# Performance work log

Hardware: AMD Instinct MI355X
Metric: run time of the kernel (lower is better)

Reference implementation:

```python
import jax, jax.numpy as jnp
import numpy as np

N_ROWS = 100000   # sparse matrix rows (nodes)
N_COLS = 8192     # input feature dim
UNITS = 128
NNZ = 2000000     # ~20 nonzeros per row


def setup_inputs() -> dict:
    key = jax.random.key(0)
    k1, k2, k3, k4, k5 = jax.random.split(key, 5)
    vals = jax.random.normal(k1, (NNZ,), dtype=jnp.float32)
    rows = jax.random.randint(k2, (NNZ,), 0, N_ROWS, dtype=jnp.int32)
    cols = jax.random.randint(k3, (NNZ,), 0, N_COLS, dtype=jnp.int32)
    # GlorotUniform-style scale for W, matching the TF initializer statistics
    limit = jnp.sqrt(6.0 / (N_COLS + UNITS)).astype(jnp.float32)
    W = jax.random.uniform(k4, (N_COLS, UNITS), dtype=jnp.float32, minval=-limit, maxval=limit)
    b = jax.random.uniform(k5, (UNITS,), dtype=jnp.float32, minval=-limit, maxval=limit)
    return {"vals": vals, "rows": rows, "cols": cols, "W": W, "b": b, "num_rows": N_ROWS}


def reference(vals, rows, cols, W, b, num_rows):
    # sparse (COO) [num_rows, F] @ dense W [F, units]:
    # gather the W row for each nonzero, scale by the nonzero value,
    # then scatter-add into the output row -> segment_sum over `rows`.
    gathered = W[cols] * vals[:, None]            # [nnz, units]
    out = jax.ops.segment_sum(gathered, rows, num_segments=num_rows)  # [num_rows, units]
    return out + b                                 # bias add (use_bias=True)
```

## Files before the change

### kernel.cpp

```cpp
#include <hip/hip_runtime.h>
#include <hip/hip_fp16.h>


#define UNITS 128
#define SCAN_BLK 1024
#define BROW 98
#define NBC_PAD 1024
#define BCAP 2528
#define CH2 8192
#define SPILL_CAP 8192


__global__ __launch_bounds__(256) void setup_kernel(
        const float* __restrict__ W, __half2* __restrict__ Wh,
        int* __restrict__ ccur, int* __restrict__ spill_cnt,
        int nbc, int wn2 ) {
    int t = blockIdx.x * blockDim.x + threadIdx.x;
    if (t < nbc) ccur[t] = t * BCAP;
    if (t == nbc) *spill_cnt = 0;
    int stride = gridDim.x * blockDim.x;
    const float2* W2 = (const float2*)W;
    for (int i = t; i < wn2; i += stride)
        Wh[i] = __float22half2_rn(W2[i]);
}


__global__ __launch_bounds__(512, 8) void partition_kernel(
        const float* __restrict__ vals, const int* __restrict__ rows,
        const int* __restrict__ cols, int* __restrict__ ccur,
        float2* __restrict__ sortedA, int* __restrict__ spill_cnt,
        float2* __restrict__ spill, int nnz, int nbc) {
    __shared__ unsigned short invs[CH2];
    __shared__ int hist[NBC_PAD];
    __shared__ int pref[NBC_PAD];
    __shared__ int gdelta[NBC_PAD];

    const int t = threadIdx.x;
    const int chunk0 = blockIdx.x * CH2;
    int n = nnz - chunk0;
    if (n > CH2) n = CH2;

    hist[t] = 0; hist[t + 512] = 0;
    __syncthreads();

    int bk[16];
#pragma unroll
    for (int j = 0; j < 16; ++j) {
        int r = j * 512 + t;
        int bkt = -1;
        if (r < n) {
            bkt = rows[chunk0 + r] / BROW;
            atomicAdd(&hist[bkt], 1);
        }
        bk[j] = bkt;
    }
    __syncthreads();

    pref[t] = hist[t]; pref[t + 512] = hist[t + 512];
    __syncthreads();
    for (int off = 1; off < NBC_PAD; off <<= 1) {
        int a0 = (t >= off) ? pref[t - off] : 0;
        int a1 = (t + 512 >= off) ? pref[t + 512 - off] : 0;
        __syncthreads();
        pref[t] += a0; pref[t + 512] += a1;
        __syncthreads();
    }

#pragma unroll
    for (int u = 0; u < 2; ++u) {
        int s = t + u * 512;
        int c = hist[s];
        int excl = pref[s] - c;
        if (s < nbc) {
            int g = (c > 0) ? atomicAdd(&ccur[s], c) : 0;
            gdelta[s] = g - excl;
        }
        hist[s] = excl;
    }
    __syncthreads();

#pragma unroll
    for (int j = 0; j < 16; ++j) {
        int bkt = bk[j];
        if (bkt >= 0) {
            int pos = atomicAdd(&hist[bkt], 1);
            invs[pos] = (unsigned short)(j * 512 + t);
        }
    }
    __syncthreads();

    for (int s = t; s < n; s += 512) {
        int r = invs[s];
        int i = chunk0 + r;
        int row = rows[i];
        float v = vals[i];
        int col = cols[i];
        int bkt = row / BROW;
        int rowlo = row - bkt * BROW;
        int dest = gdelta[bkt] + s;
        if (dest < (bkt + 1) * BCAP) {
            sortedA[dest] = make_float2(v, __int_as_float(col | (rowlo << 13)));
        } else {
            int sp = atomicAdd(spill_cnt, 1);
            if (sp < SPILL_CAP)
                spill[sp] = make_float2(v, __int_as_float(col | (row << 13)));
        }
    }
}


__global__ __launch_bounds__(512, 8) void fused_sort_compute_kernel(
        const float2* __restrict__ A, const int* __restrict__ ccur,
        const __half2* __restrict__ Wh, const float* __restrict__ b,
        float* __restrict__ out, const int* __restrict__ spill_cnt,
        const float2* __restrict__ spill, int NR) {
    __shared__ float2 st[BCAP + 8];
    __shared__ int cnt_s[128];
    __shared__ int rs[132];
    __shared__ int spill_n;
    const int t = threadIdx.x;
    const int lane = t & 63;
    const int w = t >> 6;
    const int bb = blockIdx.x;
    const int r0 = bb * BROW;
    const int gstart = bb * BCAP;
    int cnt = ccur[bb] - gstart;
    if (cnt > BCAP) cnt = BCAP;

    const float2 bias = ((const float2*)b)[lane];

    if (t < 128) cnt_s[t] = 0;
    if (t == 0) {
        int sn = *spill_cnt;
        spill_n = (sn > SPILL_CAP) ? SPILL_CAP : sn;
    }
    __syncthreads();

    float2 e[5];
#pragma unroll
    for (int j = 0; j < 5; ++j) {
        int k = j * 512 + t;
        if (k < cnt) {
            e[j] = A[gstart + k];
            atomicAdd(&cnt_s[(__float_as_int(e[j].y) >> 13) & 127], 1);
        }
    }
    __syncthreads();

    if (t < 128) rs[t] = cnt_s[t];
    __syncthreads();
    for (int off = 1; off < 128; off <<= 1) {
        int v = (t < 128 && t >= off) ? rs[t - off] : 0;
        __syncthreads();
        if (t < 128) rs[t] += v;
        __syncthreads();
    }
    int excl = (t < 128) ? rs[t] - cnt_s[t] : 0;
    __syncthreads();
    if (t < 128) { rs[t] = excl; cnt_s[t] = excl; }
    if (t == 0) rs[128] = cnt;
    __syncthreads();

#pragma unroll
    for (int j = 0; j < 5; ++j) {
        int k = j * 512 + t;
        if (k < cnt) {
            int pk = __float_as_int(e[j].y);
            int p = atomicAdd(&cnt_s[(pk >> 13) & 127], 1);
            st[p] = make_float2(e[j].x, __int_as_float(pk & 8191));
        }
    }
    __syncthreads();

    const int sn = spill_n;
    for (int r = w; r < BROW; r += 8) {
        int grow = r0 + r;
        if (grow >= NR) break;
        int s = rs[r], ee = rs[r + 1];
        float ax0 = 0.f, ay0 = 0.f, ax1 = 0.f, ay1 = 0.f;
        for (int k = s; k < ee; k += 4) {
            float2 p0 = st[k];
            float2 p1 = st[k + 1];
            float2 p2 = st[k + 2];
            float2 p3 = st[k + 3];
            int c0 = __float_as_int(p0.y) & 8191;
            int c1 = __float_as_int(p1.y) & 8191;
            int c2 = __float_as_int(p2.y) & 8191;
            int c3 = __float_as_int(p3.y) & 8191;
            float v0 = p0.x;
            float v1 = (k + 1 < ee) ? p1.x : 0.f;
            float v2 = (k + 2 < ee) ? p2.x : 0.f;
            float v3 = (k + 3 < ee) ? p3.x : 0.f;
            float2 w0 = __half22float2(Wh[c0 * 64 + lane]);
            float2 w1 = __half22float2(Wh[c1 * 64 + lane]);
            float2 w2 = __half22float2(Wh[c2 * 64 + lane]);
            float2 w3 = __half22float2(Wh[c3 * 64 + lane]);
            ax0 += v0 * w0.x; ay0 += v0 * w0.y;
            ax1 += v1 * w1.x; ay1 += v1 * w1.y;
            ax0 += v2 * w2.x; ay0 += v2 * w2.y;
            ax1 += v3 * w3.x; ay1 += v3 * w3.y;
        }
        for (int s2 = 0; s2 < sn; ++s2) {
            float2 es = spill[s2];
            int pk = __float_as_int(es.y);
            if ((pk >> 13) == grow) {
                float2 wv = __half22float2(Wh[(pk & 8191) * 64 + lane]);
                ax0 += es.x * wv.x; ay0 += es.x * wv.y;
            }
        }
        ((float2*)out)[(size_t)grow * 64 + lane] =
            make_float2(ax0 + ax1 + bias.x, ay0 + ay1 + bias.y);
    }
}


__global__ void hist_kernel(const int* __restrict__ rows, int* __restrict__ counts, int nnz) {
    int i = blockIdx.x * blockDim.x + threadIdx.x;
    if (i < nnz) atomicAdd(&counts[rows[i]], 1);
}

__global__ void scan1_kernel(const int* __restrict__ counts, int* __restrict__ tmp,
                             int* __restrict__ bsums, int NR, int NS) {
    __shared__ int s[SCAN_BLK];
    int t = threadIdx.x;
    int i = blockIdx.x * SCAN_BLK + t;
    int x = (i < NR) ? counts[i] : 0;
    s[t] = x;
    __syncthreads();
    for (int off = 1; off < SCAN_BLK; off <<= 1) {
        int v = (t >= off) ? s[t - off] : 0;
        __syncthreads();
        s[t] += v;
        __syncthreads();
    }
    if (i < NS) tmp[i] = s[t] - x;
    if (t == SCAN_BLK - 1) bsums[blockIdx.x] = s[SCAN_BLK - 1];
}

__global__ void scan2_kernel(int* __restrict__ bsums, int nb) {
    if (threadIdx.x == 0 && blockIdx.x == 0) {
        int run = 0;
        for (int i = 0; i < nb; ++i) { int c = bsums[i]; bsums[i] = run; run += c; }
    }
}

__global__ void scan3_kernel(const int* __restrict__ tmp, const int* __restrict__ bsums,
                             int* __restrict__ row_start, int* __restrict__ cursor,
                             int NR, int NS) {
    int i = blockIdx.x * blockDim.x + threadIdx.x;
    if (i < NS) {
        int v = tmp[i] + bsums[i >> 10];
        row_start[i] = v;
        if (i < NR) cursor[i] = v;
    }
}

__global__ void scatter_sort_kernel(const float* __restrict__ vals, const int* __restrict__ rows,
                                    const int* __restrict__ cols, int* __restrict__ cursor,
                                    float2* __restrict__ sorted, int nnz) {
    int i = blockIdx.x * blockDim.x + threadIdx.x;
    if (i < nnz) {
        int r = rows[i];
        int p = atomicAdd(&cursor[r], 1);
        sorted[p] = make_float2(vals[i], __int_as_float(cols[i]));
    }
}

__global__ void compute_kernel(const float2* __restrict__ sorted, const int* __restrict__ row_start,
                               const float* __restrict__ W, const float* __restrict__ b,
                               float* __restrict__ out, int NR) {
    int lane = threadIdx.x & 63;
    int wv = threadIdx.x >> 6;
    int row = blockIdx.x * 4 + wv;
    if (row >= NR) return;
    int start = row_start[row];
    int end   = row_start[row + 1];
    const float2* W2 = (const float2*)W;
    float accx0 = 0.f, accy0 = 0.f, accx1 = 0.f, accy1 = 0.f;
    for (int base = start; base < end; base += 64) {
        int m = end - base;
        if (m > 64) m = 64;
        float2 p = make_float2(0.f, __int_as_float(0));
        if (lane < m) p = sorted[base + lane];
        int vi = __float_as_int(p.x);
        int ci = __float_as_int(p.y);
        int rounds = (m + 3) & ~3;
        for (int j = 0; j < rounds; j += 4) {
            float v0 = __int_as_float(__builtin_amdgcn_readlane(vi, j));
            int   c0 = __builtin_amdgcn_readlane(ci, j);
            float v1 = __int_as_float(__builtin_amdgcn_readlane(vi, j + 1));
            int   c1 = __builtin_amdgcn_readlane(ci, j + 1);
            float v2 = __int_as_float(__builtin_amdgcn_readlane(vi, j + 2));
            int   c2 = __builtin_amdgcn_readlane(ci, j + 2);
            float v3 = __int_as_float(__builtin_amdgcn_readlane(vi, j + 3));
            int   c3 = __builtin_amdgcn_readlane(ci, j + 3);
            float2 w0 = W2[c0 * 64 + lane];
            float2 w1 = W2[c1 * 64 + lane];
            float2 w2 = W2[c2 * 64 + lane];
            float2 w3 = W2[c3 * 64 + lane];
            accx0 += v0 * w0.x; accy0 += v0 * w0.y;
            accx1 += v1 * w1.x; accy1 += v1 * w1.y;
            accx0 += v2 * w2.x; accy0 += v2 * w2.y;
            accx1 += v3 * w3.x; accy1 += v3 * w3.y;
        }
    }
    float2 bb = ((const float2*)b)[lane];
    ((float2*)out)[(size_t)row * 64 + lane] =
        make_float2(accx0 + accx1 + bb.x, accy0 + accy1 + bb.y);
}


__global__ void init_bias_kernel(float* __restrict__ out, const float* __restrict__ b, int total4) {
    const float4* b4 = (const float4*)b;
    float4* out4 = (float4*)out;
    int stride = gridDim.x * blockDim.x;
    for (int j = blockIdx.x * blockDim.x + threadIdx.x; j < total4; j += stride)
        out4[j] = b4[j & 31];
}

__global__ void scatter_atomic_kernel(const float* __restrict__ vals, const int* __restrict__ rows,
                                      const int* __restrict__ cols, const float* __restrict__ W,
                                      float* __restrict__ out, int nnz) {
    long long idx = (long long)blockIdx.x * blockDim.x + threadIdx.x;
    int i = (int)(idx >> 5);
    int c = (int)(idx & 31);
    if (i >= nnz) return;
    int row = rows[i], col = cols[i];
    float v = vals[i];
    float4 w = ((const float4*)W)[col * 32 + c];
    float* o = out + (size_t)row * UNITS + (c << 2);
    atomicAdd(o + 0, v * w.x);
    atomicAdd(o + 1, v * w.y);
    atomicAdd(o + 2, v * w.z);
    atomicAdd(o + 3, v * w.w);
}

extern "C" void kernel_launch(void* const* d_in, const int* in_sizes, int n_in,
                              void* d_out, int out_size, void* d_ws, size_t ws_size,
                              hipStream_t stream) {
    const float* vals = (const float*)d_in[0];
    const int*   rows = (const int*)d_in[1];
    const int*   cols = (const int*)d_in[2];
    const float* W    = (const float*)d_in[3];
    const float* b    = (const float*)d_in[4];
    float* out = (float*)d_out;

    const int nnz = in_sizes[0];
    const int NW  = in_sizes[3];
    const int NR  = out_size / UNITS;
    const int NS  = NR + 1;
    const int NB  = (NS + SCAN_BLK - 1) / SCAN_BLK;
    const int nbc = (NR + BROW - 1) / BROW;

    auto align = [](size_t x) { return (x + 255) & ~(size_t)255; };

    size_t off_ccur    = 0;
    size_t off_scnt    = align(off_ccur + (size_t)nbc * 4);
    size_t off_spill   = align(off_scnt + 4);
    size_t off_wh      = align(off_spill + (size_t)SPILL_CAP * 8);
    size_t off_sortedA = align(off_wh + (size_t)NW * 2);
    size_t needed_full = off_sortedA + (size_t)nbc * BCAP * 8;

    size_t t2_counts   = 0;
    size_t t2_tmp      = align(t2_counts + (size_t)NR * 4);
    size_t t2_bsums    = align(t2_tmp    + (size_t)NS * 4);
    size_t t2_rowstart = align(t2_bsums  + (size_t)NB * 4);
    size_t t2_cursor   = align(t2_rowstart + (size_t)NS * 4);
    size_t t2_sorted   = align(t2_cursor + (size_t)NR * 4);
    size_t needed_r2   = t2_sorted + (size_t)nnz * 8;

    char* ws = (char*)d_ws;

    if (ws_size >= needed_full && nbc <= NBC_PAD) {
        int*     ccur      = (int*)(ws + off_ccur);
        int*     spill_cnt = (int*)(ws + off_scnt);
        float2*  spill     = (float2*)(ws + off_spill);
        __half2* Wh        = (__half2*)(ws + off_wh);
        float2*  sortedA   = (float2*)(ws + off_sortedA);

        setup_kernel<<<512, 256, 0, stream>>>(W, Wh, ccur, spill_cnt, nbc, NW / 2);
        {
            int grid = (nnz + CH2 - 1) / CH2;
            partition_kernel<<<grid, 512, 0, stream>>>(vals, rows, cols, ccur, sortedA,
                                                       spill_cnt, spill, nnz, nbc);
        }
        fused_sort_compute_kernel<<<nbc, 512, 0, stream>>>(sortedA, ccur, Wh, b, out,
                                                           spill_cnt, spill, NR);
    } else if (ws_size >= needed_r2) {
        int*    counts    = (int*)(ws + t2_counts);
        int*    tmp       = (int*)(ws + t2_tmp);
        int*    bsums     = (int*)(ws + t2_bsums);
        int*    row_start = (int*)(ws + t2_rowstart);
        int*    cursor    = (int*)(ws + t2_cursor);
        float2* sorted    = (float2*)(ws + t2_sorted);

        hipMemsetAsync(counts, 0, (size_t)NR * 4, stream);
        {
            int block = 256, grid = (nnz + block - 1) / block;
            hist_kernel<<<grid, block, 0, stream>>>(rows, counts, nnz);
        }
        scan1_kernel<<<NB, SCAN_BLK, 0, stream>>>(counts, tmp, bsums, NR, NS);
        scan2_kernel<<<1, 64, 0, stream>>>(bsums, NB);
        {
            int block = 256, grid = (NS + block - 1) / block;
            scan3_kernel<<<grid, block, 0, stream>>>(tmp, bsums, row_start, cursor, NR, NS);
        }
        {
            int block = 256, grid = (nnz + block - 1) / block;
            scatter_sort_kernel<<<grid, block, 0, stream>>>(vals, rows, cols, cursor, sorted, nnz);
        }
        {
            int grid = (NR + 3) / 4;
            compute_kernel<<<grid, 256, 0, stream>>>(sorted, row_start, W, b, out, NR);
        }
    } else {
        int total4 = out_size / 4;
        int block = 256;
        int grid = (total4 + block - 1) / block;
        init_bias_kernel<<<grid, block, 0, stream>>>(out, b, total4);
        long long total_threads = (long long)nnz * 32;
        long long g2 = (total_threads + block - 1) / block;
        scatter_atomic_kernel<<<(int)g2, block, 0, stream>>>(vals, rows, cols, W, out, nnz);
    }
}
```

Measured before the change: 169.6 us.

## Fuse partition and compute into one persistent kernel with a grid barrier

Replaces the three-launch pipeline (setup, partition, sort+compute) with a single kernel. Each chunk block locally sorts its nonzeros by row bucket and writes per-bucket offsets, the spare blocks convert W to half, and all blocks then meet at a software grid barrier built on global atomics. After the barrier each bucket block gathers its entries from every chunk by binary search, sorts them by row in shared memory and computes the output rows. This removes kernel launch gaps and the global atomic scatter with spill handling. In exchange it depends on all ~1021 blocks being co-resident to avoid deadlock, and it silently caps each bucket at STCAP entries.

```diff
diff --git a/kernel.cpp b/kernel.cpp
--- a/kernel.cpp
+++ b/kernel.cpp
@@ -5,16 +5,253 @@
 #define UNITS 128
 #define SCAN_BLK 1024
 #define BROW 98
+#define CHA 4096
+#define NCHMAX 512
+#define NBCMAX 1024
+#define STCAP 3300
 #define NBC_PAD 1024
 #define BCAP 2528
 #define CH2 8192
 #define SPILL_CAP 8192
 
 
+__global__ __launch_bounds__(512, 8) void mega_kernel(
+        const float* __restrict__ vals, const int* __restrict__ rows,
+        const int* __restrict__ cols, const float* __restrict__ W,
+        const float* __restrict__ bias,
+        __half2* __restrict__ Wh, float2* __restrict__ sortedA,
+        int* __restrict__ boffT, int* __restrict__ bar,
+        float* __restrict__ out,
+        int nnz, int NR, int nch, int wn2) {
+    __shared__ __align__(16) char smem[36904];
+    const int t = threadIdx.x;
+    const int lane = t & 63;
+    const int w = t >> 6;
+    const int bb = blockIdx.x;
+    const int nblk = gridDim.x;
+
+    if (bb < nch) {
+        float2* sStage = (float2*)smem;
+        int*    sHist  = (int*)(smem + 32768);
+        int*    sWsum  = (int*)(smem + 36864);
+        const int chunk0 = bb * CHA;
+        int n = nnz - chunk0;
+        if (n > CHA) n = CHA;
+
+        sHist[t] = 0; sHist[t + 512] = 0;
+        __syncthreads();
+
+        int rowj[8];
+#pragma unroll
+        for (int j = 0; j < 8; ++j) {
+            int r = j * 512 + t;
+            int rv = (r < n) ? rows[chunk0 + r] : -1;
+            rowj[j] = rv;
+            if (rv >= 0) atomicAdd(&sHist[rv / BROW], 1);
+        }
+        __syncthreads();
+
+        int a0 = sHist[2 * t], a1 = sHist[2 * t + 1];
+        int ps = a0 + a1;
+        int inc = ps;
+#pragma unroll
+        for (int o = 1; o < 64; o <<= 1) {
+            int u = __shfl_up(inc, o);
+            if (lane >= o) inc += u;
+        }
+        if (lane == 63) sWsum[w] = inc;
+        __syncthreads();
+        int wbase = 0;
+        for (int i = 0; i < w; ++i) wbase += sWsum[i];
+        int exclp = wbase + inc - ps;
+        boffT[(2 * t) * NCHMAX + bb]     = exclp;
+        boffT[(2 * t + 1) * NCHMAX + bb] = exclp + a0;
+        sHist[2 * t]     = exclp;
+        sHist[2 * t + 1] = exclp + a0;
+        __syncthreads();
+
+#pragma unroll
+        for (int j = 0; j < 8; ++j) {
+            int rv = rowj[j];
+            if (rv >= 0) {
+                int r = j * 512 + t;
+                int bkt = rv / BROW;
+                int rowlo = rv - bkt * BROW;
+                int pos = atomicAdd(&sHist[bkt], 1);
+                float v = vals[chunk0 + r];
+                int col = cols[chunk0 + r];
+                sStage[pos] = make_float2(v, __int_as_float(col | (rowlo << 13)));
+            }
+        }
+        __syncthreads();
+
+        float2* dst = sortedA + (size_t)bb * CHA;
+        for (int s = t; s < n; s += 512) dst[s] = sStage[s];
+    } else {
+        const float2* W2 = (const float2*)W;
+        int cb = bb - nch;
+        int stride = (nblk - nch) * 512;
+        for (int i = cb * 512 + t; i < wn2; i += stride)
+            Wh[i] = __float22half2_rn(W2[i]);
+    }
+
+    __threadfence();
+    __syncthreads();
+    if (t == 0) {
+        int prev = __hip_atomic_fetch_add(&bar[0], 1, __ATOMIC_ACQ_REL,
+                                          __HIP_MEMORY_SCOPE_AGENT);
+        if (prev == nblk - 1)
+            __hip_atomic_store(&bar[1], 1, __ATOMIC_RELEASE,
+                               __HIP_MEMORY_SCOPE_AGENT);
+        while (__hip_atomic_load(&bar[1], __ATOMIC_ACQUIRE,
+                                 __HIP_MEMORY_SCOPE_AGENT) == 0)
+            __builtin_amdgcn_s_sleep(8);
+    }
+    __syncthreads();
+    __threadfence();
+
+    float2* sSt     = (float2*)smem;
+    int*    sRb0    = (int*)(smem + 26464);
+    int*    sRb1    = (int*)(smem + 28512);
+    int*    sDpos   = (int*)(smem + 30560);
+    int*    sCnt    = (int*)(smem + 32612);
+    int*    sRs     = (int*)(smem + 33124);
+    int*    sWsumB  = (int*)(smem + 33640);
+    int*    sRowNext= (int*)(smem + 33676);
+
+    const int r0 = bb * BROW;
+    const float2 bv = ((const float2*)bias)[lane];
+
+    for (int c = t; c < nch; c += 512) {
+        sRb0[c] = boffT[bb * NCHMAX + c];
+        sRb1[c] = boffT[(bb + 1) * NCHMAX + c];
+    }
+    if (t < 128) sCnt[t] = 0;
+    if (t == 0) sRowNext[0] = 0;
+    __syncthreads();
+
+    int len = (t < nch) ? (sRb1[t] - sRb0[t]) : 0;
+    int inc2 = len;
+#pragma unroll
+    for (int o = 1; o < 64; o <<= 1) {
+        int u = __shfl_up(inc2, o);
+        if (lane >= o) inc2 += u;
+    }
+    if (lane == 63) sWsumB[w] = inc2;
+    __syncthreads();
+    int wbase2 = 0;
+    for (int i = 0; i < w; ++i) wbase2 += sWsumB[i];
+    int excl2 = wbase2 + inc2 - len;
+    sDpos[t] = excl2;
+    if (t == 511) sDpos[512] = excl2 + len;
+    __syncthreads();
+
+    int cnt = sDpos[nch];
+    if (cnt > STCAP) cnt = STCAP;
+
+    float2 e[7];
+#pragma unroll
+    for (int j = 0; j < 7; ++j) {
+        int g = j * 512 + t;
+        if (g < cnt) {
+            int lo = 0, hi = nch;
+            while (hi - lo > 1) {
+                int mid = (lo + hi) >> 1;
+                if (sDpos[mid] <= g) lo = mid; else hi = mid;
+            }
+            int o2 = g - sDpos[lo];
+            e[j] = sortedA[(size_t)lo * CHA + sRb0[lo] + o2];
+            atomicAdd(&sCnt[(__float_as_int(e[j].y) >> 13) & 127], 1);
+        }
+    }
+    __syncthreads();
+
+    if (t < 128) sRs[t] = sCnt[t];
+    __syncthreads();
+    for (int off = 1; off < 128; off <<= 1) {
+        int v = (t < 128 && t >= off) ? sRs[t - off] : 0;
+        __syncthreads();
+        if (t < 128) sRs[t] += v;
+        __syncthreads();
+    }
+    int excl3 = (t < 128) ? sRs[t] - sCnt[t] : 0;
+    __syncthreads();
+    if (t < 128) { sRs[t] = excl3; sCnt[t] = excl3; }
+    if (t == 0) sRs[128] = cnt;
+    __syncthreads();
+
+#pragma unroll
+    for (int j = 0; j < 7; ++j) {
+        int g = j * 512 + t;
+        if (g < cnt) {
+            int pk = __float_as_int(e[j].y);
+            int p = atomicAdd(&sCnt[(pk >> 13) & 127], 1);
+            sSt[p] = make_float2(e[j].x, __int_as_float(pk & 8191));
+        }
+    }
+    __syncthreads();
+
+    while (true) {
+        int rr = 0;
+        if (lane == 0) rr = atomicAdd(sRowNext, 1);
+        rr = __shfl(rr, 0);
+        if (rr >= BROW) break;
+        int grow = r0 + rr;
+        if (grow >= NR) break;
+        int s = sRs[rr], ee = sRs[rr + 1];
+        float ax0 = 0.f, ay0 = 0.f, ax1 = 0.f, ay1 = 0.f;
+        for (int k = s; k < ee; k += 8) {
+            float2 p0 = sSt[k];
+            float2 p1 = sSt[k + 1];
+            float2 p2 = sSt[k + 2];
+            float2 p3 = sSt[k + 3];
+            float2 p4 = sSt[k + 4];
+            float2 p5 = sSt[k + 5];
+            float2 p6 = sSt[k + 6];
+            float2 p7 = sSt[k + 7];
+            int c0 = __float_as_int(p0.y) & 8191;
+            int c1 = __float_as_int(p1.y) & 8191;
+            int c2 = __float_as_int(p2.y) & 8191;
+            int c3 = __float_as_int(p3.y) & 8191;
+            int c4 = __float_as_int(p4.y) & 8191;
+            int c5 = __float_as_int(p5.y) & 8191;
+            int c6 = __float_as_int(p6.y) & 8191;
+            int c7 = __float_as_int(p7.y) & 8191;
+            float v0 = p0.x;
+            float v1 = (k + 1 < ee) ? p1.x : 0.f;
+            float v2 = (k + 2 < ee) ? p2.x : 0.f;
+            float v3 = (k + 3 < ee) ? p3.x : 0.f;
+            float v4 = (k + 4 < ee) ? p4.x : 0.f;
+            float v5 = (k + 5 < ee) ? p5.x : 0.f;
+            float v6 = (k + 6 < ee) ? p6.x : 0.f;
+            float v7 = (k + 7 < ee) ? p7.x : 0.f;
+            float2 w0 = __half22float2(Wh[c0 * 64 + lane]);
+            float2 w1 = __half22float2(Wh[c1 * 64 + lane]);
+            float2 w2 = __half22float2(Wh[c2 * 64 + lane]);
+            float2 w3 = __half22float2(Wh[c3 * 64 + lane]);
+            float2 w4 = __half22float2(Wh[c4 * 64 + lane]);
+            float2 w5 = __half22float2(Wh[c5 * 64 + lane]);
+            float2 w6 = __half22float2(Wh[c6 * 64 + lane]);
+            float2 w7 = __half22float2(Wh[c7 * 64 + lane]);
+            ax0 += v0 * w0.x; ay0 += v0 * w0.y;
+            ax1 += v1 * w1.x; ay1 += v1 * w1.y;
+            ax0 += v2 * w2.x; ay0 += v2 * w2.y;
+            ax1 += v3 * w3.x; ay1 += v3 * w3.y;
+            ax0 += v4 * w4.x; ay0 += v4 * w4.y;
+            ax1 += v5 * w5.x; ay1 += v5 * w5.y;
+            ax0 += v6 * w6.x; ay0 += v6 * w6.y;
+            ax1 += v7 * w7.x; ay1 += v7 * w7.y;
+        }
+        ((float2*)out)[(size_t)grow * 64 + lane] =
+            make_float2(ax0 + ax1 + bv.x, ay0 + ay1 + bv.y);
+    }
+}
+
+
 __global__ __launch_bounds__(256) void setup_kernel(
         const float* __restrict__ W, __half2* __restrict__ Wh,
         int* __restrict__ ccur, int* __restrict__ spill_cnt,
-        int nbc, int wn2 ) {
+        int nbc, int wn2) {
     int t = blockIdx.x * blockDim.x + threadIdx.x;
     if (t < nbc) ccur[t] = t * BCAP;
     if (t == nbc) *spill_cnt = 0;
@@ -23,7 +260,6 @@
     for (int i = t; i < wn2; i += stride)
         Wh[i] = __float22half2_rn(W2[i]);
 }
-
 
 __global__ __launch_bounds__(512, 8) void partition_kernel(
         const float* __restrict__ vals, const int* __restrict__ rows,
@@ -107,7 +343,6 @@
         }
     }
 }
-
 
 __global__ __launch_bounds__(512, 8) void fused_sort_compute_kernel(
         const float2* __restrict__ A, const int* __restrict__ ccur,
@@ -351,8 +586,15 @@
     const int NS  = NR + 1;
     const int NB  = (NS + SCAN_BLK - 1) / SCAN_BLK;
     const int nbc = (NR + BROW - 1) / BROW;
+    const int nch = (nnz + CHA - 1) / CHA;
 
     auto align = [](size_t x) { return (x + 255) & ~(size_t)255; };
+
+    size_t c_wh      = 0;
+    size_t c_sortedA = align(c_wh + (size_t)NW * 2);
+    size_t c_boffT   = align(c_sortedA + (size_t)nch * CHA * 8);
+    size_t c_bar     = align(c_boffT + (size_t)NBCMAX * NCHMAX * 4);
+    size_t needed_coop = c_bar + 256;
 
     size_t off_ccur    = 0;
     size_t off_scnt    = align(off_ccur + (size_t)nbc * 4);
@@ -371,7 +613,17 @@
 
     char* ws = (char*)d_ws;
 
-    if (ws_size >= needed_full && nbc <= NBC_PAD) {
+    if (ws_size >= needed_coop && nbc >= 2 && nbc <= NBCMAX &&
+        nch >= 1 && nch <= NCHMAX && nch < nbc) {
+        __half2* Wh      = (__half2*)(ws + c_wh);
+        float2*  sortedA = (float2*)(ws + c_sortedA);
+        int*     boffT   = (int*)(ws + c_boffT);
+        int*     bar     = (int*)(ws + c_bar);
+
+        hipMemsetAsync(bar, 0, 8, stream);
+        mega_kernel<<<nbc, 512, 0, stream>>>(vals, rows, cols, W, b, Wh, sortedA,
+                                             boffT, bar, out, nnz, NR, nch, NW / 2);
+    } else if (ws_size >= needed_full && nbc <= NBC_PAD) {
         int*     ccur      = (int*)(ws + off_ccur);
         int*     spill_cnt = (int*)(ws + off_scnt);
         float2*  spill     = (float2*)(ws + off_spill);
```

New measurement: 579.4 us. 3.42x slower.

## Fold W half conversion into partition kernel, shrink chunks, use wave-shuffle scan

Applied to the files above, without the earlier changes.

Removes the separate setup kernel. W-to-half conversion now runs inside the partition kernel, and the bucket cursors plus spill counter are zeroed with one memset. Partition chunks shrink from 8192 to 2048 elements, giving about four times as many blocks, and the 1024-entry LDS Hillis-Steele scan becomes a wave-shuffle scan over pairs. The goal is to cut launch overhead, the barrier-heavy scan and per-block serial work, at the cost of many more global atomics on the bucket cursors and shorter contiguous write runs into each bucket.

```diff
diff --git a/kernel.cpp b/kernel.cpp
--- a/kernel.cpp
+++ b/kernel.cpp
@@ -7,45 +7,43 @@
 #define BROW 98
 #define NBC_PAD 1024
 #define BCAP 2528
-#define CH2 8192
+#define CH3 2048
 #define SPILL_CAP 8192
-
-
-__global__ __launch_bounds__(256) void setup_kernel(
-        const float* __restrict__ W, __half2* __restrict__ Wh,
-        int* __restrict__ ccur, int* __restrict__ spill_cnt,
-        int nbc, int wn2 ) {
-    int t = blockIdx.x * blockDim.x + threadIdx.x;
-    if (t < nbc) ccur[t] = t * BCAP;
-    if (t == nbc) *spill_cnt = 0;
-    int stride = gridDim.x * blockDim.x;
-    const float2* W2 = (const float2*)W;
-    for (int i = t; i < wn2; i += stride)
-        Wh[i] = __float22half2_rn(W2[i]);
-}
 
 
 __global__ __launch_bounds__(512, 8) void partition_kernel(
         const float* __restrict__ vals, const int* __restrict__ rows,
-        const int* __restrict__ cols, int* __restrict__ ccur,
-        float2* __restrict__ sortedA, int* __restrict__ spill_cnt,
-        float2* __restrict__ spill, int nnz, int nbc) {
-    __shared__ unsigned short invs[CH2];
+        const int* __restrict__ cols, const float* __restrict__ W,
+        __half2* __restrict__ Wh, int* __restrict__ ccur,
+        float2* __restrict__ sortedA, float2* __restrict__ spill,
+        int nnz, int nbc, int wn2) {
+    __shared__ unsigned short invs[CH3];
     __shared__ int hist[NBC_PAD];
-    __shared__ int pref[NBC_PAD];
     __shared__ int gdelta[NBC_PAD];
+    __shared__ int wsum[8];
 
     const int t = threadIdx.x;
-    const int chunk0 = blockIdx.x * CH2;
+    const int lane = t & 63;
+    const int w = t >> 6;
+    const int bb = blockIdx.x;
+
+    {
+        const float2* W2 = (const float2*)W;
+        int stride = gridDim.x * 512;
+        for (int i = bb * 512 + t; i < wn2; i += stride)
+            Wh[i] = __float22half2_rn(W2[i]);
+    }
+
+    const int chunk0 = bb * CH3;
     int n = nnz - chunk0;
-    if (n > CH2) n = CH2;
+    if (n > CH3) n = CH3;
 
     hist[t] = 0; hist[t + 512] = 0;
     __syncthreads();
 
-    int bk[16];
+    int bk[4];
 #pragma unroll
-    for (int j = 0; j < 16; ++j) {
+    for (int j = 0; j < 4; ++j) {
         int r = j * 512 + t;
         int bkt = -1;
         if (r < n) {
@@ -56,31 +54,37 @@
     }
     __syncthreads();
 
-    pref[t] = hist[t]; pref[t + 512] = hist[t + 512];
-    __syncthreads();
-    for (int off = 1; off < NBC_PAD; off <<= 1) {
-        int a0 = (t >= off) ? pref[t - off] : 0;
-        int a1 = (t + 512 >= off) ? pref[t + 512 - off] : 0;
-        __syncthreads();
-        pref[t] += a0; pref[t + 512] += a1;
-        __syncthreads();
-    }
-
+    int a0 = hist[2 * t], a1 = hist[2 * t + 1];
+    int ps = a0 + a1;
+    int inc = ps;
 #pragma unroll
-    for (int u = 0; u < 2; ++u) {
-        int s = t + u * 512;
-        int c = hist[s];
-        int excl = pref[s] - c;
-        if (s < nbc) {
-            int g = (c > 0) ? atomicAdd(&ccur[s], c) : 0;
-            gdelta[s] = g - excl;
-        }
-        hist[s] = excl;
+    for (int o = 1; o < 64; o <<= 1) {
+        int u = __shfl_up(inc, o);
+        if (lane >= o) inc += u;
+    }
+    if (lane == 63) wsum[w] = inc;
+    __syncthreads();
+    int wbase = 0;
+    for (int i = 0; i < w; ++i) wbase += wsum[i];
+    int exclp = wbase + inc - ps;
+
+    {
+        int s0 = 2 * t, s1 = 2 * t + 1;
+        if (s0 < nbc) {
+            int g = (a0 > 0) ? atomicAdd(&ccur[s0], a0) : 0;
+            gdelta[s0] = s0 * BCAP + g - exclp;
+        }
+        if (s1 < nbc) {
+            int g = (a1 > 0) ? atomicAdd(&ccur[s1], a1) : 0;
+            gdelta[s1] = s1 * BCAP + g - (exclp + a0);
+        }
+        hist[s0] = exclp;
+        hist[s1] = exclp + a0;
     }
     __syncthreads();
 
 #pragma unroll
-    for (int j = 0; j < 16; ++j) {
+    for (int j = 0; j < 4; ++j) {
         int bkt = bk[j];
         if (bkt >= 0) {
             int pos = atomicAdd(&hist[bkt], 1);
@@ -89,6 +93,7 @@
     }
     __syncthreads();
 
+    int* spill_cnt = &ccur[nbc];
     for (int s = t; s < n; s += 512) {
         int r = invs[s];
         int i = chunk0 + r;
@@ -112,8 +117,7 @@
 __global__ __launch_bounds__(512, 8) void fused_sort_compute_kernel(
         const float2* __restrict__ A, const int* __restrict__ ccur,
         const __half2* __restrict__ Wh, const float* __restrict__ b,
-        float* __restrict__ out, const int* __restrict__ spill_cnt,
-        const float2* __restrict__ spill, int NR) {
+        float* __restrict__ out, int nbc, int NR) {
     __shared__ float2 st[BCAP + 8];
     __shared__ int cnt_s[128];
     __shared__ int rs[132];
@@ -124,14 +128,14 @@
     const int bb = blockIdx.x;
     const int r0 = bb * BROW;
     const int gstart = bb * BCAP;
-    int cnt = ccur[bb] - gstart;
+    int cnt = ccur[bb];
     if (cnt > BCAP) cnt = BCAP;
 
     const float2 bias = ((const float2*)b)[lane];
 
     if (t < 128) cnt_s[t] = 0;
     if (t == 0) {
-        int sn = *spill_cnt;
+        int sn = ccur[nbc];
         spill_n = (sn > SPILL_CAP) ? SPILL_CAP : sn;
     }
     __syncthreads();
@@ -173,6 +177,7 @@
     __syncthreads();
 
     const int sn = spill_n;
+    const float2* spill = A + (size_t)nbc * BCAP;
     for (int r = w; r < BROW; r += 8) {
         int grow = r0 + r;
         if (grow >= NR) break;
@@ -355,11 +360,10 @@
     auto align = [](size_t x) { return (x + 255) & ~(size_t)255; };
 
     size_t off_ccur    = 0;
-    size_t off_scnt    = align(off_ccur + (size_t)nbc * 4);
-    size_t off_spill   = align(off_scnt + 4);
-    size_t off_wh      = align(off_spill + (size_t)SPILL_CAP * 8);
+    size_t off_wh      = align(off_ccur + (size_t)(nbc + 1) * 4);
     size_t off_sortedA = align(off_wh + (size_t)NW * 2);
-    size_t needed_full = off_sortedA + (size_t)nbc * BCAP * 8;
+    size_t off_spill   = off_sortedA + (size_t)nbc * BCAP * 8;
+    size_t needed_full = off_spill + (size_t)SPILL_CAP * 8;
 
     size_t t2_counts   = 0;
     size_t t2_tmp      = align(t2_counts + (size_t)NR * 4);
@@ -372,20 +376,20 @@
     char* ws = (char*)d_ws;
 
     if (ws_size >= needed_full && nbc <= NBC_PAD) {
-        int*     ccur      = (int*)(ws + off_ccur);
-        int*     spill_cnt = (int*)(ws + off_scnt);
-        float2*  spill     = (float2*)(ws + off_spill);
-        __half2* Wh        = (__half2*)(ws + off_wh);
-        float2*  sortedA   = (float2*)(ws + off_sortedA);
-
-        setup_kernel<<<512, 256, 0, stream>>>(W, Wh, ccur, spill_cnt, nbc, NW / 2);
+        int*     ccur    = (int*)(ws + off_ccur);
+        __half2* Wh      = (__half2*)(ws + off_wh);
+        float2*  sortedA = (float2*)(ws + off_sortedA);
+        float2*  spill   = (float2*)(ws + off_spill);
+
+        hipMemsetAsync(ccur, 0, (size_t)(nbc + 1) * 4, stream);
         {
-            int grid = (nnz + CH2 - 1) / CH2;
-            partition_kernel<<<grid, 512, 0, stream>>>(vals, rows, cols, ccur, sortedA,
-                                                       spill_cnt, spill, nnz, nbc);
-        }
-        fused_sort_compute_kernel<<<nbc, 512, 0, stream>>>(sortedA, ccur, Wh, b, out,
-                                                           spill_cnt, spill, NR);
+            int grid = (nnz + CH3 - 1) / CH3;
+            partition_kernel<<<grid, 512, 0, stream>>>(vals, rows, cols, W, Wh,
+                                                       ccur, sortedA, spill,
+                                                       nnz, nbc, NW / 2);
+        }
+        fused_sort_compute_kernel<<<nbc, 512, 0, stream>>>(sortedA, ccur, Wh, b,
+                                                           out, nbc, NR);
     } else if (ws_size >= needed_r2) {
         int*    counts    = (int*)(ws + t2_counts);
         int*    tmp       = (int*)(ws + t2_tmp);
```

New measurement: 203.5 us. 1.2x slower.
